# Performance work log

Hardware: AMD Instinct MI355X
Metric: run time of the kernel (lower is better)

Reference implementation:

```python
import jax, jax.numpy as jnp
import numpy as np

K_TAPS = 4

def batch_lsigf(h, S, x, b):
    """h: [Gout,E,K,Fin], S: [B,E,N,N], x: [B,Fin,N], b: [Gout,1] -> [B,Gout,N]."""
    Gout, E, K, Fin = h.shape
    B, _, _, N = S.shape
    xk = jnp.broadcast_to(x[:, None], (B, E, Fin, N))  # tap k=0
    taps = [xk]
    for _ in range(1, K):
        xk = jnp.matmul(xk, S)  # [B,E,Fin,N] @ [B,E,N,N]
        taps.append(xk)
    z = jnp.stack(taps, axis=2)  # [B,E,K,Fin,N]
    y = jnp.einsum('bekfn,gekf->bgn', z, h)
    if b is not None:
        y = y + b  # [Gout,1] broadcasts over nodes
    return y

def setup_inputs() -> dict:
    key = jax.random.key(0)
    ks = jax.random.split(key, 9)
    B, N = 16, 1024
    G = F = H = 128
    E, K = 1, K_TAPS
    sa = 1.0 / np.sqrt(G * K)
    sb = 1.0 / np.sqrt(H * K)
    return {
        'x': jax.random.normal(ks[0], (B, G, N), jnp.float32),
        'hidden': jax.random.normal(ks[1], (B, H, N), jnp.float32),
        'S': jax.random.normal(ks[2], (B, E, N, N), jnp.float32) / np.sqrt(N),
        'weight_A': jax.random.uniform(ks[3], (H, E, K, G), jnp.float32, -sa, sa),
        'weight_B': jax.random.uniform(ks[4], (H, E, K, H), jnp.float32, -sb, sb),
        'weight_D': jax.random.uniform(ks[5], (F, E, K, H), jnp.float32, -sb, sb),
        'bias_A': jax.random.uniform(ks[6], (H, 1), jnp.float32, -sa, sa),
        'bias_B': jax.random.uniform(ks[7], (H, 1), jnp.float32, -sb, sb),
        'bias_D': jax.random.uniform(ks[8], (F, 1), jnp.float32, -sb, sb),
    }

def reference(x, hidden, S, weight_A, weight_B, weight_D, bias_A, bias_B, bias_D):
    u_a = batch_lsigf(weight_A, S, x, bias_A)        # input path
    u_b = batch_lsigf(weight_B, S, hidden, bias_B)   # recurrent path
    h_next = jax.nn.relu(u_a + u_b)                  # new hidden state
    u = batch_lsigf(weight_D, S, h_next, bias_D)     # output projection
    return u
```

## Files before the change

kernel.cpp:

```cpp
#include <hip/hip_runtime.h>


typedef __attribute__((ext_vector_type(8))) short short8;
typedef __attribute__((ext_vector_type(4))) float floatx4;

#define AS1 __attribute__((address_space(1)))
#define AS3 __attribute__((address_space(3)))

__device__ __forceinline__ unsigned short f2bf(float f) {
  union { float f; unsigned u; } v; v.f = f;
  unsigned r = v.u + 0x7fffu + ((v.u >> 16) & 1u);
  return (unsigned short)(r >> 16);
}
__device__ __forceinline__ float bf2f(unsigned short b) {
  union { unsigned u; float f; } v; v.u = ((unsigned)b) << 16;
  return v.f;
}

__device__ __forceinline__ void gload16(const void* g, void* l) {
  __builtin_amdgcn_global_load_lds((const AS1 void*)g, (AS3 void*)l, 16, 0, 0);
}

template<int EPI>
__global__ __launch_bounds__(256, 3)
void gemm_bt(const unsigned short* __restrict__ A, long long aBatch, int lda,
             const unsigned short* __restrict__ Bt, long long bBatch, int ldb,
             int K,
             const unsigned short* __restrict__ cinit, long long ciBatch,
             const float* __restrict__ bias,
             unsigned short* __restrict__ outb, long long obBatch,
             float* __restrict__ outf, long long ofBatch,
             unsigned short* __restrict__ mixv, long long mvBatch)
{
  constexpr int MT   = (EPI == 3) ? 8 : 2;
  constexpr int PERB = 16 * MT;
  __shared__ unsigned short buf[3][128 * 64];

  const int wg  = blockIdx.x;
  const int xcd = wg & 7;
  const int idx = wg >> 3;
  const int b   = xcd * 2 + idx / PERB;
  const int r   = idx % PERB;
  const int n0  = (r & 15) * 64;
  const int m0  = (r >> 4) * 64;

  const int tid  = threadIdx.x;
  const int wave = tid >> 6;
  const int lane = tid & 63;
  const int wr   = (wave >> 1) * 32;
  const int wc   = (wave & 1) * 32;
  const int l15  = lane & 15;
  const int lhi  = lane >> 4;

  const unsigned short* Ab = A + (long long)b * aBatch;
  const unsigned short* Bb = Bt + (long long)b * bBatch;

  floatx4 acc[2][2];
  #pragma unroll
  for (int mi = 0; mi < 2; ++mi)
    #pragma unroll
    for (int ni = 0; ni < 2; ++ni)
      acc[mi][ni] = (floatx4){0.f, 0.f, 0.f, 0.f};

  auto stage = [&](int slot, int k0) {
    #pragma unroll
    for (int i = 0; i < 4; ++i) {
      const int u  = wave * 4 + i;
      const int q  = u * 64 + lane;
      const int rr = q >> 3;
      const int c8 = ((q & 7) ^ (rr & 7)) * 8;
      const unsigned short* src = (rr < 64)
          ? Ab + (long long)(m0 + rr) * lda + k0 + c8
          : Bb + (long long)(n0 + rr - 64) * ldb + k0 + c8;
      gload16(src, &buf[slot][u * 512]);
    }
  };

  const int NT = K >> 6;
  stage(0, 0);
  if (NT > 1) stage(1, 64);

  for (int t = 0; t < NT; ++t) {
    if (t + 1 < NT) { asm volatile("s_waitcnt vmcnt(4)" ::: "memory"); }
    else            { asm volatile("s_waitcnt vmcnt(0)" ::: "memory"); }
    __builtin_amdgcn_s_barrier();
    __builtin_amdgcn_sched_barrier(0);
    if (t + 2 < NT) stage((t + 2) % 3, (t + 2) * 64);

    const unsigned short* bp = &buf[t % 3][0];
    #pragma unroll
    for (int kk = 0; kk < 2; ++kk) {
      short8 af[2], bv[2];
      #pragma unroll
      for (int mi = 0; mi < 2; ++mi) {
        const int row = wr + mi * 16 + l15;
        af[mi] = *(const short8*)(&bp[row * 64 + (((kk * 4 + lhi) ^ (row & 7)) << 3)]);
      }
      #pragma unroll
      for (int ni = 0; ni < 2; ++ni) {
        const int row = 64 + wc + ni * 16 + l15;
        bv[ni] = *(const short8*)(&bp[row * 64 + (((kk * 4 + lhi) ^ (row & 7)) << 3)]);
      }
      #pragma unroll
      for (int mi = 0; mi < 2; ++mi)
        #pragma unroll
        for (int ni = 0; ni < 2; ++ni)
          acc[mi][ni] = __builtin_amdgcn_mfma_f32_16x16x32_bf16(af[mi], bv[ni], acc[mi][ni], 0, 0, 0);
    }
  }

  if (EPI == 0) {
    const unsigned short* ci = cinit + (long long)b * ciBatch;
    unsigned short* ob = outb + (long long)b * obBatch;
    #pragma unroll
    for (int mi = 0; mi < 2; ++mi)
      #pragma unroll
      for (int ni = 0; ni < 2; ++ni)
        #pragma unroll
        for (int j = 0; j < 4; ++j) {
          const int row = m0 + wr + mi * 16 + lhi * 4 + j;
          const int col = n0 + wc + ni * 16 + l15;
          ob[(long long)row * 1024 + col] =
              f2bf(acc[mi][ni][j] + bf2f(ci[(long long)row * 1024 + col]));
        }
  } else if (EPI == 2) {
    const unsigned short* ci = cinit + (long long)b * ciBatch;
    float* of = outf + (long long)b * ofBatch;
    #pragma unroll
    for (int mi = 0; mi < 2; ++mi)
      #pragma unroll
      for (int ni = 0; ni < 2; ++ni)
        #pragma unroll
        for (int j = 0; j < 4; ++j) {
          const int row = m0 + wr + mi * 16 + lhi * 4 + j;
          const int col = n0 + wc + ni * 16 + l15;
          of[(long long)row * 1024 + col] =
              acc[mi][ni][j] + bf2f(ci[(long long)row * 1024 + col]);
        }
  } else if (EPI == 3) {
    #pragma unroll
    for (int mi = 0; mi < 2; ++mi)
      #pragma unroll
      for (int ni = 0; ni < 2; ++ni)
        #pragma unroll
        for (int j = 0; j < 4; ++j) {
          const int gr = m0 + wr + mi * 16 + lhi * 4 + j;
          const int kc = gr >> 7;
          const int rl = gr & 127;
          const int col = n0 + wc + ni * 16 + l15;
          unsigned short* dst = (kc == 3) ? (mixv + (long long)b * mvBatch)
                                          : (outb + (long long)b * obBatch + kc * (128 * 1024));
          float v = acc[mi][ni][j];
          if (kc == 0 && bias != nullptr) v += bias[rl];
          dst[(long long)rl * 1024 + col] = f2bf(v);
        }
  } else {
    const unsigned short* ci = cinit + (long long)b * ciBatch;
    __syncthreads();
    unsigned short (*tt)[72] = (unsigned short(*)[72])(&buf[0][0]);
    #pragma unroll
    for (int mi = 0; mi < 2; ++mi)
      #pragma unroll
      for (int ni = 0; ni < 2; ++ni)
        #pragma unroll
        for (int j = 0; j < 4; ++j) {
          const int rowl = wr + mi * 16 + lhi * 4 + j;
          const int coll = wc + ni * 16 + l15;
          float v = acc[mi][ni][j] +
                    bf2f(ci[(long long)(m0 + rowl) * 1024 + n0 + coll]);
          tt[coll][rowl] = f2bf(fmaxf(v, 0.f));
        }
    __syncthreads();
    unsigned short* ob = outb + (long long)b * obBatch;
    #pragma unroll
    for (int i = 0; i < 2; ++i) {
      const int flat = tid + i * 256;
      const int node = flat >> 3;
      const int seg  = flat & 7;
      *(short8*)(&ob[(long long)(n0 + node) * 128 + m0 + seg * 8]) =
          *(const short8*)(&tt[node][seg * 8]);
    }
  }
}

__global__ __launch_bounds__(256)
void transpose_S(const float* __restrict__ in, unsigned short* __restrict__ out)
{
  __shared__ float t[64][65];
  const int b  = blockIdx.z;
  const int c0 = blockIdx.x * 64;
  const int r0 = blockIdx.y * 64;
  const int tx = threadIdx.x & 63;
  const int ty = threadIdx.x >> 6;
  const float* ib = in + (long long)b * (1024 * 1024);
  unsigned short* ob = out + (long long)b * (1024 * 1024);
  #pragma unroll
  for (int i = 0; i < 64; i += 4)
    t[ty + i][tx] = ib[(long long)(r0 + ty + i) * 1024 + c0 + tx];
  __syncthreads();
  #pragma unroll
  for (int i = 0; i < 64; i += 4)
    ob[(long long)(c0 + ty + i) * 1024 + r0 + tx] = f2bf(t[tx][ty + i]);
}

__global__ __launch_bounds__(256)
void transpose_xh(const float* __restrict__ x, const float* __restrict__ h,
                  unsigned short* __restrict__ z0t)
{
  __shared__ float t[64][65];
  const int z  = blockIdx.z;
  const int b  = z & 15;
  const float* src = (z < 16) ? (x + (long long)b * (128 * 1024))
                              : (h + (long long)b * (128 * 1024));
  const int colOff = (z < 16) ? 0 : 128;
  const int c0 = blockIdx.x * 64;
  const int r0 = blockIdx.y * 64;
  const int tx = threadIdx.x & 63;
  const int ty = threadIdx.x >> 6;
  #pragma unroll
  for (int i = 0; i < 64; i += 4)
    t[ty + i][tx] = src[(long long)(r0 + ty + i) * 1024 + c0 + tx];
  __syncthreads();
  unsigned short* ob = z0t + (long long)b * (1024 * 256);
  #pragma unroll
  for (int i = 0; i < 64; i += 4)
    ob[(long long)(c0 + ty + i) * 256 + colOff + r0 + tx] = f2bf(t[tx][ty + i]);
}

__global__ __launch_bounds__(256)
void prep_weights(const float* __restrict__ wA, const float* __restrict__ wB,
                  const float* __restrict__ wD,
                  const float* __restrict__ bA, const float* __restrict__ bB,
                  unsigned short* __restrict__ W1, unsigned short* __restrict__ W2,
                  float* __restrict__ biasAB)
{
  const int i = blockIdx.x * 256 + threadIdx.x;
  if (i < 512 * 256) {
    const int row = i >> 8, g2 = i & 255;
    const int k = row >> 7, h = row & 127;
    const float v = (g2 < 128) ? wA[(h * 4 + k) * 128 + g2]
                               : wB[(h * 4 + k) * 128 + (g2 - 128)];
    W1[i] = f2bf(v);
  }
  const int j = i - 512 * 256;
  if (j >= 0 && j < 512 * 128) {
    const int row = j >> 7, h2 = j & 127;
    const int k = row >> 7, f = row & 127;
    W2[j] = f2bf(wD[(f * 4 + k) * 128 + h2]);
  }
  const int l = i - 512 * 256 - 512 * 128;
  if (l >= 0 && l < 128) biasAB[l] = bA[l] + bB[l];
}

extern "C" void kernel_launch(void* const* d_in, const int* in_sizes, int n_in,
                              void* d_out, int out_size, void* d_ws, size_t ws_size,
                              hipStream_t stream)
{
  const float* x   = (const float*)d_in[0];
  const float* hid = (const float*)d_in[1];
  const float* S   = (const float*)d_in[2];
  const float* wA  = (const float*)d_in[3];
  const float* wB  = (const float*)d_in[4];
  const float* wD  = (const float*)d_in[5];
  const float* bA  = (const float*)d_in[6];
  const float* bB  = (const float*)d_in[7];
  const float* bD  = (const float*)d_in[8];
  float* out = (float*)d_out;

  char* ws = (char*)d_ws;
  auto alloc = [&](size_t bytes) {
    char* p = ws;
    ws += (bytes + 255) & ~(size_t)255;
    return p;
  };
  unsigned short* St   = (unsigned short*)alloc(16ull * 1024 * 1024 * 2);
  unsigned short* z0t  = (unsigned short*)alloc(16ull * 1024 * 256 * 2);
  unsigned short* cini = (unsigned short*)alloc(16ull * 3 * 128 * 1024 * 2);
  unsigned short* vb0  = (unsigned short*)alloc(16ull * 128 * 1024 * 2);
  unsigned short* vb1  = (unsigned short*)alloc(16ull * 128 * 1024 * 2);
  unsigned short* hnt  = (unsigned short*)alloc(16ull * 1024 * 128 * 2);
  unsigned short* W1   = (unsigned short*)alloc(512 * 256 * 2);
  unsigned short* W2   = (unsigned short*)alloc(512 * 128 * 2);
  float*          bAB  = (float*)alloc(128 * 4);

  const long long NB  = 128 * 1024;
  const long long NB2 = 1024 * 128;
  const long long CI  = 3 * NB;
  const long long SB  = 1024 * 1024;

  prep_weights<<<dim3(769), 256, 0, stream>>>(wA, wB, wD, bA, bB, W1, W2, bAB);
  transpose_S<<<dim3(16, 16, 16), 256, 0, stream>>>(S, St);
  transpose_xh<<<dim3(16, 2, 32), 256, 0, stream>>>(x, hid, z0t);

  gemm_bt<3><<<dim3(2048), 256, 0, stream>>>(W1, 0, 256, z0t, 1024 * 256, 256, 256,
      nullptr, 0, bAB, cini, CI, nullptr, 0, vb0, NB);
  gemm_bt<0><<<dim3(512), 256, 0, stream>>>(vb0, NB, 1024, St, SB, 1024, 1024,
      cini + 2 * NB, CI, nullptr, vb1, NB, nullptr, 0, nullptr, 0);
  gemm_bt<0><<<dim3(512), 256, 0, stream>>>(vb1, NB, 1024, St, SB, 1024, 1024,
      cini + 1 * NB, CI, nullptr, vb0, NB, nullptr, 0, nullptr, 0);
  gemm_bt<4><<<dim3(512), 256, 0, stream>>>(vb0, NB, 1024, St, SB, 1024, 1024,
      cini, CI, nullptr, hnt, NB2, nullptr, 0, nullptr, 0);

  gemm_bt<3><<<dim3(2048), 256, 0, stream>>>(W2, 0, 128, hnt, NB2, 128, 128,
      nullptr, 0, bD, cini, CI, nullptr, 0, vb0, NB);
  gemm_bt<0><<<dim3(512), 256, 0, stream>>>(vb0, NB, 1024, St, SB, 1024, 1024,
      cini + 2 * NB, CI, nullptr, vb1, NB, nullptr, 0, nullptr, 0);
  gemm_bt<0><<<dim3(512), 256, 0, stream>>>(vb1, NB, 1024, St, SB, 1024, 1024,
      cini + 1 * NB, CI, nullptr, vb0, NB, nullptr, 0, nullptr, 0);
  gemm_bt<2><<<dim3(512), 256, 0, stream>>>(vb0, NB, 1024, St, SB, 1024, 1024,
      cini, CI, nullptr, nullptr, 0, out, NB, nullptr, 0);
}
```

Measured before the change: 111.3 us.

## Deepen GEMM pipeline to four LDS stages and fuse prep kernels into one

The GEMM K loop length becomes a compile-time template parameter. The loop is now fully unrolled with a four-slot LDS ring (prefetch distance 3) in place of three slots. Global source pointers and LDS fragment offsets are precomputed once, and s_setprio is raised around the MFMA groups. The three preprocessing kernels (weight repack, S transpose, x/h transpose) are merged into one launch that walks several tiles per workgroup. The aim is to hide more memory latency, cut address arithmetic and save two kernel launches, in exchange for more LDS per workgroup and lower occupancy (launch bound 3→2).

```diff
diff --git a/kernel.cpp b/kernel.cpp
--- a/kernel.cpp
+++ b/kernel.cpp
@@ -21,20 +21,20 @@
   __builtin_amdgcn_global_load_lds((const AS1 void*)g, (AS3 void*)l, 16, 0, 0);
 }
 
-template<int EPI>
-__global__ __launch_bounds__(256, 3)
+template<int EPI, int KK>
+__global__ __launch_bounds__(256, 2)
 void gemm_bt(const unsigned short* __restrict__ A, long long aBatch, int lda,
              const unsigned short* __restrict__ Bt, long long bBatch, int ldb,
-             int K,
              const unsigned short* __restrict__ cinit, long long ciBatch,
              const float* __restrict__ bias,
              unsigned short* __restrict__ outb, long long obBatch,
              float* __restrict__ outf, long long ofBatch,
              unsigned short* __restrict__ mixv, long long mvBatch)
 {
+  constexpr int NT   = KK / 64;
   constexpr int MT   = (EPI == 3) ? 8 : 2;
   constexpr int PERB = 16 * MT;
-  __shared__ unsigned short buf[3][128 * 64];
+  __shared__ unsigned short buf[4][128 * 64];
 
   const int wg  = blockIdx.x;
   const int xcd = wg & 7;
@@ -55,6 +55,36 @@
   const unsigned short* Ab = A + (long long)b * aBatch;
   const unsigned short* Bb = Bt + (long long)b * bBatch;
 
+  const unsigned short* src[4];
+  int ldsoff[4];
+  #pragma unroll
+  for (int i = 0; i < 4; ++i) {
+    const int u  = wave * 4 + i;
+    const int rr = u * 8 + (lane >> 3);
+    const int c8 = ((lane & 7) ^ (rr & 7)) * 8;
+    src[i] = (rr < 64) ? Ab + (long long)(m0 + rr) * lda + c8
+                       : Bb + (long long)(n0 + rr - 64) * ldb + c8;
+    ldsoff[i] = u * 512;
+  }
+  auto stage = [&](int slot) {
+    #pragma unroll
+    for (int i = 0; i < 4; ++i) {
+      gload16(src[i], &buf[slot][ldsoff[i]]);
+      src[i] += 64;
+    }
+  };
+
+  int aoff[2][2], boff[2][2];
+  #pragma unroll
+  for (int mi = 0; mi < 2; ++mi)
+    #pragma unroll
+    for (int kk = 0; kk < 2; ++kk) {
+      const int rowa = wr + mi * 16 + l15;
+      aoff[kk][mi] = rowa * 64 + (((kk * 4 + lhi) ^ (rowa & 7)) << 3);
+      const int rowb = 64 + wc + mi * 16 + l15;
+      boff[kk][mi] = rowb * 64 + (((kk * 4 + lhi) ^ (rowb & 7)) << 3);
+    }
+
   floatx4 acc[2][2];
   #pragma unroll
   for (int mi = 0; mi < 2; ++mi)
@@ -62,50 +92,35 @@
     for (int ni = 0; ni < 2; ++ni)
       acc[mi][ni] = (floatx4){0.f, 0.f, 0.f, 0.f};
 
-  auto stage = [&](int slot, int k0) {
-    #pragma unroll
-    for (int i = 0; i < 4; ++i) {
-      const int u  = wave * 4 + i;
-      const int q  = u * 64 + lane;
-      const int rr = q >> 3;
-      const int c8 = ((q & 7) ^ (rr & 7)) * 8;
-      const unsigned short* src = (rr < 64)
-          ? Ab + (long long)(m0 + rr) * lda + k0 + c8
-          : Bb + (long long)(n0 + rr - 64) * ldb + k0 + c8;
-      gload16(src, &buf[slot][u * 512]);
-    }
-  };
-
-  const int NT = K >> 6;
-  stage(0, 0);
-  if (NT > 1) stage(1, 64);
-
+  stage(0);
+  if (NT > 1) stage(1);
+  if (NT > 2) stage(2);
+
+  #pragma unroll
   for (int t = 0; t < NT; ++t) {
-    if (t + 1 < NT) { asm volatile("s_waitcnt vmcnt(4)" ::: "memory"); }
-    else            { asm volatile("s_waitcnt vmcnt(0)" ::: "memory"); }
+    const int rem = NT - 1 - t;
+    if (rem >= 2)      { asm volatile("s_waitcnt vmcnt(8)" ::: "memory"); }
+    else if (rem == 1) { asm volatile("s_waitcnt vmcnt(4)" ::: "memory"); }
+    else               { asm volatile("s_waitcnt vmcnt(0)" ::: "memory"); }
     __builtin_amdgcn_s_barrier();
     __builtin_amdgcn_sched_barrier(0);
-    if (t + 2 < NT) stage((t + 2) % 3, (t + 2) * 64);
-
-    const unsigned short* bp = &buf[t % 3][0];
+    if (t + 3 < NT) stage((t + 3) & 3);
+
+    const unsigned short* bp = &buf[t & 3][0];
     #pragma unroll
     for (int kk = 0; kk < 2; ++kk) {
       short8 af[2], bv[2];
       #pragma unroll
-      for (int mi = 0; mi < 2; ++mi) {
-        const int row = wr + mi * 16 + l15;
-        af[mi] = *(const short8*)(&bp[row * 64 + (((kk * 4 + lhi) ^ (row & 7)) << 3)]);
-      }
-      #pragma unroll
-      for (int ni = 0; ni < 2; ++ni) {
-        const int row = 64 + wc + ni * 16 + l15;
-        bv[ni] = *(const short8*)(&bp[row * 64 + (((kk * 4 + lhi) ^ (row & 7)) << 3)]);
-      }
+      for (int mi = 0; mi < 2; ++mi) af[mi] = *(const short8*)(bp + aoff[kk][mi]);
+      #pragma unroll
+      for (int ni = 0; ni < 2; ++ni) bv[ni] = *(const short8*)(bp + boff[kk][ni]);
+      __builtin_amdgcn_s_setprio(1);
       #pragma unroll
       for (int mi = 0; mi < 2; ++mi)
         #pragma unroll
         for (int ni = 0; ni < 2; ++ni)
           acc[mi][ni] = __builtin_amdgcn_mfma_f32_16x16x32_bf16(af[mi], bv[ni], acc[mi][ni], 0, 0, 0);
+      __builtin_amdgcn_s_setprio(0);
     }
   }
 
@@ -184,72 +199,75 @@
 }
 
 __global__ __launch_bounds__(256)
-void transpose_S(const float* __restrict__ in, unsigned short* __restrict__ out)
+void prep_all(const float* __restrict__ x, const float* __restrict__ hid,
+              const float* __restrict__ S,
+              const float* __restrict__ wA, const float* __restrict__ wB,
+              const float* __restrict__ wD,
+              const float* __restrict__ bA, const float* __restrict__ bB,
+              unsigned short* __restrict__ St, unsigned short* __restrict__ z0t,
+              unsigned short* __restrict__ W1, unsigned short* __restrict__ W2,
+              float* __restrict__ biasAB)
 {
   __shared__ float t[64][65];
-  const int b  = blockIdx.z;
-  const int c0 = blockIdx.x * 64;
-  const int r0 = blockIdx.y * 64;
-  const int tx = threadIdx.x & 63;
-  const int ty = threadIdx.x >> 6;
-  const float* ib = in + (long long)b * (1024 * 1024);
-  unsigned short* ob = out + (long long)b * (1024 * 1024);
-  #pragma unroll
-  for (int i = 0; i < 64; i += 4)
-    t[ty + i][tx] = ib[(long long)(r0 + ty + i) * 1024 + c0 + tx];
-  __syncthreads();
-  #pragma unroll
-  for (int i = 0; i < 64; i += 4)
-    ob[(long long)(c0 + ty + i) * 1024 + r0 + tx] = f2bf(t[tx][ty + i]);
-}
-
-__global__ __launch_bounds__(256)
-void transpose_xh(const float* __restrict__ x, const float* __restrict__ h,
-                  unsigned short* __restrict__ z0t)
-{
-  __shared__ float t[64][65];
-  const int z  = blockIdx.z;
-  const int b  = z & 15;
-  const float* src = (z < 16) ? (x + (long long)b * (128 * 1024))
-                              : (h + (long long)b * (128 * 1024));
-  const int colOff = (z < 16) ? 0 : 128;
-  const int c0 = blockIdx.x * 64;
-  const int r0 = blockIdx.y * 64;
-  const int tx = threadIdx.x & 63;
-  const int ty = threadIdx.x >> 6;
-  #pragma unroll
-  for (int i = 0; i < 64; i += 4)
-    t[ty + i][tx] = src[(long long)(r0 + ty + i) * 1024 + c0 + tx];
-  __syncthreads();
-  unsigned short* ob = z0t + (long long)b * (1024 * 256);
-  #pragma unroll
-  for (int i = 0; i < 64; i += 4)
-    ob[(long long)(c0 + ty + i) * 256 + colOff + r0 + tx] = f2bf(t[tx][ty + i]);
-}
-
-__global__ __launch_bounds__(256)
-void prep_weights(const float* __restrict__ wA, const float* __restrict__ wB,
-                  const float* __restrict__ wD,
-                  const float* __restrict__ bA, const float* __restrict__ bB,
-                  unsigned short* __restrict__ W1, unsigned short* __restrict__ W2,
-                  float* __restrict__ biasAB)
-{
-  const int i = blockIdx.x * 256 + threadIdx.x;
-  if (i < 512 * 256) {
-    const int row = i >> 8, g2 = i & 255;
-    const int k = row >> 7, h = row & 127;
-    const float v = (g2 < 128) ? wA[(h * 4 + k) * 128 + g2]
-                               : wB[(h * 4 + k) * 128 + (g2 - 128)];
-    W1[i] = f2bf(v);
-  }
-  const int j = i - 512 * 256;
-  if (j >= 0 && j < 512 * 128) {
-    const int row = j >> 7, h2 = j & 127;
-    const int k = row >> 7, f = row & 127;
-    W2[j] = f2bf(wD[(f * 4 + k) * 128 + h2]);
-  }
-  const int l = i - 512 * 256 - 512 * 128;
-  if (l >= 0 && l < 128) biasAB[l] = bA[l] + bB[l];
+  const int wg  = blockIdx.x;
+  const int tid = threadIdx.x;
+
+  #pragma unroll
+  for (int k = 0; k < 2; ++k) {
+    const int i = wg * 512 + k * 256 + tid;
+    if (i < 512 * 256) {
+      const int row = i >> 8, g2 = i & 255;
+      const int kk = row >> 7, h = row & 127;
+      const float v = (g2 < 128) ? wA[(h * 4 + kk) * 128 + g2]
+                                 : wB[(h * 4 + kk) * 128 + (g2 - 128)];
+      W1[i] = f2bf(v);
+    } else if (i < 512 * 256 + 512 * 128) {
+      const int j = i - 512 * 256;
+      const int row = j >> 7, h2 = j & 127;
+      const int kk = row >> 7, f = row & 127;
+      W2[j] = f2bf(wD[(f * 4 + kk) * 128 + h2]);
+    } else if (i < 512 * 256 + 512 * 128 + 128) {
+      const int l = i - 512 * 256 - 512 * 128;
+      biasAB[l] = bA[l] + bB[l];
+    }
+  }
+
+  const int b  = (wg & 7) * 2 + (wg >> 3) / 32;
+  const int jj = (wg >> 3) % 32;
+  const int tx = tid & 63;
+  const int ty = tid >> 6;
+
+  const float* Sb = S + (long long)b * (1024 * 1024);
+  unsigned short* Stb = St + (long long)b * (1024 * 1024);
+  for (int q = 0; q < 8; ++q) {
+    const int tile = jj * 8 + q;
+    const int c0 = (tile & 15) * 64, r0 = (tile >> 4) * 64;
+    __syncthreads();
+    #pragma unroll
+    for (int i = 0; i < 64; i += 4)
+      t[ty + i][tx] = Sb[(r0 + ty + i) * 1024 + c0 + tx];
+    __syncthreads();
+    #pragma unroll
+    for (int i = 0; i < 64; i += 4)
+      Stb[(long long)(c0 + ty + i) * 1024 + r0 + tx] = f2bf(t[tx][ty + i]);
+  }
+
+  unsigned short* zb = z0t + (long long)b * (1024 * 256);
+  for (int q = 0; q < 2; ++q) {
+    const int idx2 = jj * 2 + q;
+    const int srch = idx2 >> 5;
+    const int t2   = idx2 & 31;
+    const int c0 = (t2 & 15) * 64, r0 = ((t2 >> 4) & 1) * 64;
+    const float* sp = (srch ? hid : x) + (long long)b * (128 * 1024);
+    __syncthreads();
+    #pragma unroll
+    for (int i = 0; i < 64; i += 4)
+      t[ty + i][tx] = sp[(r0 + ty + i) * 1024 + c0 + tx];
+    __syncthreads();
+    #pragma unroll
+    for (int i = 0; i < 64; i += 4)
+      zb[(long long)(c0 + ty + i) * 256 + srch * 128 + r0 + tx] = f2bf(t[tx][ty + i]);
+  }
 }
 
 extern "C" void kernel_launch(void* const* d_in, const int* in_sizes, int n_in,
@@ -288,25 +306,24 @@
   const long long CI  = 3 * NB;
   const long long SB  = 1024 * 1024;
 
-  prep_weights<<<dim3(769), 256, 0, stream>>>(wA, wB, wD, bA, bB, W1, W2, bAB);
-  transpose_S<<<dim3(16, 16, 16), 256, 0, stream>>>(S, St);
-  transpose_xh<<<dim3(16, 2, 32), 256, 0, stream>>>(x, hid, z0t);
-
-  gemm_bt<3><<<dim3(2048), 256, 0, stream>>>(W1, 0, 256, z0t, 1024 * 256, 256, 256,
+  prep_all<<<dim3(512), 256, 0, stream>>>(x, hid, S, wA, wB, wD, bA, bB,
+                                          St, z0t, W1, W2, bAB);
+
+  gemm_bt<3, 256><<<dim3(2048), 256, 0, stream>>>(W1, 0, 256, z0t, 1024 * 256, 256,
       nullptr, 0, bAB, cini, CI, nullptr, 0, vb0, NB);
-  gemm_bt<0><<<dim3(512), 256, 0, stream>>>(vb0, NB, 1024, St, SB, 1024, 1024,
+  gemm_bt<0, 1024><<<dim3(512), 256, 0, stream>>>(vb0, NB, 1024, St, SB, 1024,
       cini + 2 * NB, CI, nullptr, vb1, NB, nullptr, 0, nullptr, 0);
-  gemm_bt<0><<<dim3(512), 256, 0, stream>>>(vb1, NB, 1024, St, SB, 1024, 1024,
+  gemm_bt<0, 1024><<<dim3(512), 256, 0, stream>>>(vb1, NB, 1024, St, SB, 1024,
       cini + 1 * NB, CI, nullptr, vb0, NB, nullptr, 0, nullptr, 0);
-  gemm_bt<4><<<dim3(512), 256, 0, stream>>>(vb0, NB, 1024, St, SB, 1024, 1024,
+  gemm_bt<4, 1024><<<dim3(512), 256, 0, stream>>>(vb0, NB, 1024, St, SB, 1024,
       cini, CI, nullptr, hnt, NB2, nullptr, 0, nullptr, 0);
 
-  gemm_bt<3><<<dim3(2048), 256, 0, stream>>>(W2, 0, 128, hnt, NB2, 128, 128,
+  gemm_bt<3, 128><<<dim3(2048), 256, 0, stream>>>(W2, 0, 128, hnt, NB2, 128,
       nullptr, 0, bD, cini, CI, nullptr, 0, vb0, NB);
-  gemm_bt<0><<<dim3(512), 256, 0, stream>>>(vb0, NB, 1024, St, SB, 1024, 1024,
+  gemm_bt<0, 1024><<<dim3(512), 256, 0, stream>>>(vb0, NB, 1024, St, SB, 1024,
       cini + 2 * NB, CI, nullptr, vb1, NB, nullptr, 0, nullptr, 0);
-  gemm_bt<0><<<dim3(512), 256, 0, stream>>>(vb1, NB, 1024, St, SB, 1024, 1024,
+  gemm_bt<0, 1024><<<dim3(512), 256, 0, stream>>>(vb1, NB, 1024, St, SB, 1024,
       cini + 1 * NB, CI, nullptr, vb0, NB, nullptr, 0, nullptr, 0);
-  gemm_bt<2><<<dim3(512), 256, 0, stream>>>(vb0, NB, 1024, St, SB, 1024, 1024,
+  gemm_bt<2, 1024><<<dim3(512), 256, 0, stream>>>(vb0, NB, 1024, St, SB, 1024,
       cini, CI, nullptr, nullptr, 0, out, NB, nullptr, 0);
 }
```

New measurement: 107.3 us. -3.6%, faster.
